# Optimization experiments

Measured on AMD Instinct MI355X. Metric: run time of the kernel, lower is better.

The kernel has to match this reference:

```python
import jax, jax.numpy as jnp
import numpy as np

N = 100000
E = 3200000
C = 32
EPS = 1e-5
SLOPE = 0.01  # nn.LeakyReLU default negative slope


def _param_key(i):
    return jax.random.fold_in(jax.random.key(42), i)


def setup_inputs() -> dict:
    key = jax.random.key(0)
    k0, k1, k2, k3 = jax.random.split(key, 4)
    patch_embs = jax.random.normal(k0, (N, C), jnp.float32)
    row = jax.random.randint(k1, (E,), 0, N)
    off = jax.random.randint(k2, (E,), 1, N)
    col = (row + off) % N  # guarantees no self loops (PyG removes+re-adds them)
    edge_index = jnp.stack([row, col]).astype(jnp.int64)
    edge_attr = jax.random.normal(k3, (E, 1), jnp.float32)
    s = 1.0 / np.sqrt(C)
    inp = {"patch_embs": patch_embs, "edge_index": edge_index, "edge_attr": edge_attr}
    for i in (1, 2, 3):
        ka, kb = jax.random.split(_param_key(i))
        inp[f"W{i}_out"] = jax.random.uniform(ka, (C, C), jnp.float32, -s, s)
        inp[f"b{i}_out"] = jnp.zeros((C,), jnp.float32)
        inp[f"W{i}_root"] = jax.random.uniform(kb, (C, C), jnp.float32, -s, s)
        inp[f"g{i}"] = jnp.ones((C,), jnp.float32)
        inp[f"be{i}"] = jnp.zeros((C,), jnp.float32)
    return inp


def _cluster_gcn(x, row, col, W_out, b_out, W_root):
    n = x.shape[0]
    loops = jnp.arange(n, dtype=row.dtype)
    r = jnp.concatenate([row, loops])
    c = jnp.concatenate([col, loops])
    deg = jax.ops.segment_sum(jnp.ones_like(c, jnp.float32), c, num_segments=n)
    deg_inv = 1.0 / jnp.clip(deg, 1.0)  # degree(col).clamp_(1.)
    w = deg_inv[c]  # diag_lambda = 0 default
    agg = jax.ops.segment_sum(x[r] * w[:, None], c, num_segments=n)
    return agg @ W_out + b_out + x @ W_root


def _bn_train(x, g, b):
    m = jnp.mean(x, axis=0)
    v = jnp.mean(jnp.square(x - m), axis=0)  # biased var, BatchNorm1d training
    return (x - m) * jax.lax.rsqrt(v + EPS) * g + b


def _leaky(x):
    return jnp.where(x >= 0, x, SLOPE * x)


def reference(patch_embs, edge_index, edge_attr,
              W1_out, b1_out, W1_root, g1, be1,
              W2_out, b2_out, W2_root, g2, be2,
              W3_out, b3_out, W3_root, g3, be3):
    row, col = edge_index[0], edge_index[1]
    x = _bn_train(_leaky(_cluster_gcn(patch_embs, row, col, W1_out, b1_out, W1_root)) + patch_embs, g1, be1)
    x = _bn_train(_leaky(_cluster_gcn(x, row, col, W2_out, b2_out, W2_root)) + x, g2, be2)
    x = _bn_train(_cluster_gcn(x, row, col, W3_out, b3_out, W3_root) + x, g3, be3)
    return x
```

## Files before the change

### kernel.cpp

```cpp
#include <hip/hip_runtime.h>
#include <hip/hip_fp8.h>

#define SLOPE 0.01f
#define BN_EPS 1e-5f
#define CH 32
#define GATHER_BLOCKS 3125
#define DENSE_BLOCKS 1024
#define APPLY_BLOCKS 1024
#define SLOTS 80

#define BSH 8
#define BNODES 256
#define NBMAX 512

#if defined(__has_builtin)
#if __has_builtin(__builtin_amdgcn_cvt_pk_f32_fp8)
#define USE_CVT_PK 1
#endif
#endif

typedef float v2f __attribute__((ext_vector_type(2)));
typedef float v4f __attribute__((ext_vector_type(4)));

static __device__ __forceinline__ float q2f(unsigned char b) {
    __hip_fp8_e4m3 t;
    t.__x = (__hip_fp8_storage_t)b;
    return (float)t;
}
static __device__ __forceinline__ unsigned char f2q(float f) {
    __hip_fp8_e4m3 t(f);
    return (unsigned char)t.__x;
}
static __device__ __forceinline__ unsigned short f2bf(float f) {
    unsigned int x = __float_as_uint(f);
    x += 0x7fffu + ((x >> 16) & 1u);
    return (unsigned short)(x >> 16);
}
static __device__ __forceinline__ float bf2f(unsigned int u16) {
    return __uint_as_float(u16 << 16);
}
static __device__ __forceinline__ void dec_add(unsigned int u, float4& a) {
#ifdef USE_CVT_PK
    v2f lo = __builtin_amdgcn_cvt_pk_f32_fp8((int)u, false);
    v2f hi = __builtin_amdgcn_cvt_pk_f32_fp8((int)u, true);
    a.x += lo.x; a.y += lo.y; a.z += hi.x; a.w += hi.y;
#else
    a.x += q2f((unsigned char)(u & 0xff));
    a.y += q2f((unsigned char)((u >> 8) & 0xff));
    a.z += q2f((unsigned char)((u >> 16) & 0xff));
    a.w += q2f((unsigned char)(u >> 24));
#endif
}
static __device__ __forceinline__ void nt_store4(const float4& a, float4* p) {
    v4f t; t.x = a.x; t.y = a.y; t.z = a.z; t.w = a.w;
    __builtin_nontemporal_store(t, (v4f*)p);
}

static __device__ __forceinline__ void fin_body(const float* __restrict__ partials,
        int nprt, const float* __restrict__ g, const float* __restrict__ be,
        float* __restrict__ stO, int nv) {
    __shared__ float4 red4[16][16];
    __shared__ double sdv[64];
    int tid = threadIdx.x;
    const float4* p4 = (const float4*)partials;
    int col4 = tid & 15, grp = tid >> 4;
    float4 s = make_float4(0.f, 0.f, 0.f, 0.f);
    for (int r = grp; r < nprt; r += 16) {
        float4 t = p4[(size_t)r * 16 + col4];
        s.x += t.x; s.y += t.y; s.z += t.z; s.w += t.w;
    }
    red4[grp][col4] = s;
    __syncthreads();
    if (tid < 64) {
        int c4 = tid >> 2, cc = tid & 3;
        double tot = 0.0;
#pragma unroll
        for (int k = 0; k < 16; ++k) {
            const float* rr = (const float*)&red4[k][c4];
            tot += (double)rr[cc];
        }
        sdv[tid] = tot;
    }
    __syncthreads();
    if (tid < 32) {
        double mean = sdv[tid] / (double)nv;
        double var  = sdv[32 + tid] / (double)nv - mean * mean;
        float inv = rsqrtf(fmaxf((float)var, 0.f) + BN_EPS);
        float scv = g[tid] * inv;
        stO[tid] = scv;
        stO[32 + tid] = be[tid] - (float)mean * scv;
    }
}


__global__ __launch_bounds__(256) void cast_hist_kernel(
        const float4* __restrict__ x4, unsigned int* __restrict__ xq4, int n4,
        const int* __restrict__ col, int* __restrict__ ghist, int nE, int nb,
        float* __restrict__ st0) {
    __shared__ int h[NBMAX];
    for (int i = threadIdx.x; i < nb; i += 256) h[i] = 0;
    __syncthreads();
    int gt = blockIdx.x * 256 + threadIdx.x, gs = gridDim.x * 256;
    for (int e = gt; e < nE; e += gs)
        atomicAdd(&h[col[e] >> BSH], 1);
    for (int i = gt; i < n4; i += gs) {
        float4 v = x4[i];
        unsigned int o = (unsigned int)f2q(v.x)
                       | ((unsigned int)f2q(v.y) << 8)
                       | ((unsigned int)f2q(v.z) << 16)
                       | ((unsigned int)f2q(v.w) << 24);
        xq4[i] = o;
    }
    if (blockIdx.x == 0) {
        if (threadIdx.x < 64)
            st0[threadIdx.x] = (threadIdx.x < 32) ? 1.0f : 0.0f;
        if (threadIdx.x < 8)
            xq4[n4 + threadIdx.x] = 0u;
    }
    __syncthreads();
    for (int i = threadIdx.x; i < nb; i += 256) {
        int v = h[i];
        if (v) atomicAdd(&ghist[i], v);
    }
}

__global__ __launch_bounds__(512) void bscan_kernel(const int* __restrict__ ghist,
        int* __restrict__ bbase, int* __restrict__ gcur, int nb) {
    __shared__ int sh[512];
    int tid = threadIdx.x;
    int v = (tid < nb) ? ghist[tid] : 0;
    sh[tid] = v;
    __syncthreads();
    int acc = v;
#pragma unroll
    for (int d = 1; d < 512; d <<= 1) {
        int t = (tid >= d) ? sh[tid - d] : 0;
        __syncthreads();
        acc += t;
        sh[tid] = acc;
        __syncthreads();
    }
    int excl = acc - v;
    if (tid < nb) { bbase[tid] = excl; gcur[tid] = excl; }
    if (tid == nb - 1) bbase[nb] = acc;
}

__global__ __launch_bounds__(1024) void part_kernel(const int* __restrict__ row,
        const int* __restrict__ col, int* __restrict__ gcur,
        unsigned int* __restrict__ staging, int nE, int nb) {
    __shared__ int hist[NBMAX], gb[NBMAX], lcur[NBMAX];
    int tid = threadIdx.x;
    for (int i = tid; i < nb; i += 1024) hist[i] = 0;
    __syncthreads();
    int base = blockIdx.x * 8192;
    int r[8], bk[8];
    unsigned int lo[8];
    bool ok[8];
#pragma unroll
    for (int k = 0; k < 8; ++k) {
        int e = base + (k << 10) + tid;
        ok[k] = (e < nE);
        if (ok[k]) {
            int rr = row[e], cc = col[e];
            r[k] = rr; bk[k] = cc >> BSH; lo[k] = (unsigned)(cc & (BNODES - 1));
            atomicAdd(&hist[bk[k]], 1);
        }
    }
    __syncthreads();
    for (int i = tid; i < nb; i += 1024) {
        int h = hist[i];
        if (h) gb[i] = atomicAdd(&gcur[i], h);
        lcur[i] = 0;
    }
    __syncthreads();
#pragma unroll
    for (int k = 0; k < 8; ++k) {
        if (ok[k]) {
            int b = bk[k];
            int p = gb[b] + atomicAdd(&lcur[b], 1);
            staging[p] = ((unsigned)r[k] << BSH) | lo[k];
        }
    }
}

__global__ __launch_bounds__(256) void build_kernel(const unsigned int* __restrict__ staging,
        const int* __restrict__ bbase, int* __restrict__ adj, int* __restrict__ pdeg,
        float* __restrict__ dinv, int n, int zoff) {
    int b = blockIdx.x;
    int b0 = b << BSH;
    int tid = threadIdx.x;
    int es = bbase[b], ee = bbase[b + 1];
    __shared__ int cnt[BNODES];
    cnt[tid] = 0;
    __syncthreads();
    for (int i = es + tid; i < ee; i += 256)
        atomicAdd(&cnt[staging[i] & (BNODES - 1)], 1);
    __syncthreads();
    int node = b0 + tid;
    int d = cnt[tid];
    if (node < n) {
        dinv[node] = 1.0f / (float)(d + 1);
        int pd = (d + 15) & ~15;
        if (pd > SLOTS) pd = SLOTS;
        pdeg[node] = pd;
        int ab = node * SLOTS;
        for (int s2 = d; s2 < pd; ++s2) adj[ab + s2] = zoff;
    }
    cnt[tid] = 0;
    __syncthreads();
    for (int i = es + tid; i < ee; i += 256) {
        unsigned int wv = staging[i];
        int c = wv & (BNODES - 1);
        int p = atomicAdd(&cnt[c], 1);
        if (p < SLOTS)
            adj[(b0 + c) * SLOTS + p] = (int)(wv >> BSH) * CH;
    }
}


__global__ __launch_bounds__(256, 4) void gather_kernel(
        const unsigned char* __restrict__ xq,
        const int* __restrict__ pdeg, const int* __restrict__ adj,
        float4* __restrict__ S4, int n,
        const float* __restrict__ partials, int nprt,
        const float* __restrict__ g, const float* __restrict__ be,
        float* __restrict__ st_out) {
    if (blockIdx.x >= GATHER_BLOCKS) {
        if (partials) fin_body(partials, nprt, g, be, st_out, n);
        return;
    }
    int tid = threadIdx.x;
    int lane = tid & 63, w = tid >> 6;
    int h = lane >> 5;
    int q = (lane & 31) >> 2;
    int r8 = (lane & 3) * 8;
    int half = (blockIdx.x * 4 + w) * 2 + h;
    int nH = GATHER_BLOCKS * 8;
    for (int base = half * 4; base < n; base += nH * 4) {
        int v0 = base, v1 = base + 1, v2 = base + 2, v3 = base + 3;
        int j0 = v0 * SLOTS, j1 = v1 * SLOTS, j2 = v2 * SLOTS, j3 = v3 * SLOTS;
        int e0 = j0 + pdeg[v0];
        int e1 = (v1 < n) ? j1 + pdeg[v1] : j1;
        int e2 = (v2 < n) ? j2 + pdeg[v2] : j2;
        int e3 = (v3 < n) ? j3 + pdeg[v3] : j3;
        float4 c0A = {0,0,0,0}, c0B = {0,0,0,0};
        float4 c1A = {0,0,0,0}, c1B = {0,0,0,0};
        float4 c2A = {0,0,0,0}, c2B = {0,0,0,0};
        float4 c3A = {0,0,0,0}, c3B = {0,0,0,0};
#define LD16(k) int aA##k = adj[j##k + q]; int aB##k = adj[j##k + 8 + q];
#define GD16(k) uint2 uA##k = *(const uint2*)(xq + aA##k + r8); \
                uint2 uB##k = *(const uint2*)(xq + aB##k + r8);
#define AC16(k) dec_add(uA##k.x, c##k##A); dec_add(uA##k.y, c##k##B); \
                dec_add(uB##k.x, c##k##A); dec_add(uB##k.y, c##k##B); j##k += 16;
        while (j0 < e0 && j1 < e1 && j2 < e2 && j3 < e3) {
            LD16(0) LD16(1) LD16(2) LD16(3)
            GD16(0) GD16(1) GD16(2) GD16(3)
            AC16(0) AC16(1) AC16(2) AC16(3)
        }
        while (j0 < e0 && j1 < e1) { LD16(0) LD16(1) GD16(0) GD16(1) AC16(0) AC16(1) }
        while (j2 < e2 && j3 < e3) { LD16(2) LD16(3) GD16(2) GD16(3) AC16(2) AC16(3) }
        while (j0 < e0) { LD16(0) GD16(0) AC16(0) }
        while (j1 < e1) { LD16(1) GD16(1) AC16(1) }
        while (j2 < e2) { LD16(2) GD16(2) AC16(2) }
        while (j3 < e3) { LD16(3) GD16(3) AC16(3) }
#undef LD16
#undef GD16
#undef AC16
#define MRG4(a, m) a.x += __shfl_xor(a.x, m); a.y += __shfl_xor(a.y, m); \
                   a.z += __shfl_xor(a.z, m); a.w += __shfl_xor(a.w, m);
        MRG4(c0A, 4)  MRG4(c0B, 4)  MRG4(c1A, 4)  MRG4(c1B, 4)
        MRG4(c2A, 4)  MRG4(c2B, 4)  MRG4(c3A, 4)  MRG4(c3B, 4)
        MRG4(c0A, 8)  MRG4(c0B, 8)  MRG4(c1A, 8)  MRG4(c1B, 8)
        MRG4(c2A, 8)  MRG4(c2B, 8)  MRG4(c3A, 8)  MRG4(c3B, 8)
        MRG4(c0A, 16) MRG4(c0B, 16) MRG4(c1A, 16) MRG4(c1B, 16)
        MRG4(c2A, 16) MRG4(c2B, 16) MRG4(c3A, 16) MRG4(c3B, 16)
#undef MRG4
        if (q == 0) {
            int r2 = r8 >> 2;
            nt_store4(c0A, &S4[(size_t)v0 * 8 + r2]);
            nt_store4(c0B, &S4[(size_t)v0 * 8 + r2 + 1]);
            if (v1 < n) { nt_store4(c1A, &S4[(size_t)v1 * 8 + r2]);
                          nt_store4(c1B, &S4[(size_t)v1 * 8 + r2 + 1]); }
            if (v2 < n) { nt_store4(c2A, &S4[(size_t)v2 * 8 + r2]);
                          nt_store4(c2B, &S4[(size_t)v2 * 8 + r2 + 1]); }
            if (v3 < n) { nt_store4(c3A, &S4[(size_t)v3 * 8 + r2]);
                          nt_store4(c3B, &S4[(size_t)v3 * 8 + r2 + 1]); }
        }
    }
}


__global__ __launch_bounds__(256) void dense_kernel(
        const float* __restrict__ zin, float* __restrict__ Sz,
        const float* __restrict__ dinv, const float* __restrict__ st,
        const float* __restrict__ Wout, const float* __restrict__ bout,
        const float* __restrict__ Wroot,
        float* __restrict__ partials, unsigned int* __restrict__ zq4,
        int n, int do_leaky) {
    __shared__ float2 WI[CH * CH];
    __shared__ float red[2][4][CH];
    int tid = threadIdx.x;
    for (int i = tid; i < CH * CH; i += 256)
        WI[i] = make_float2(Wout[i], Wroot[i]);
    __syncthreads();
    int lane = tid & 63, w = tid >> 6;
    int c = lane & 31, h = lane >> 5;
    float bo = bout[c];
    float sc = st[c], sh = st[32 + c];
    int hw0 = (blockIdx.x * 4 + w) * 2 + h;
    int nHW = gridDim.x * 8;
    float bsum = 0.f, bsq = 0.f;
    for (int v = hw0; v < n; v += nHW) {
        float Sv = Sz[(size_t)v * CH + c];
        float zv = zin[(size_t)v * CH + c];
        float xv = fmaf(sc, zv, sh);
        float a = fmaf(sc * (Sv + zv), dinv[v], sh);
        unsigned int pk = (unsigned int)f2bf(a) | ((unsigned int)f2bf(xv) << 16);
        float2 acc0 = {0.f, 0.f}, acc1 = {0.f, 0.f};
        float2 acc2 = {0.f, 0.f}, acc3 = {0.f, 0.f};
#pragma unroll
        for (int k = 0; k < CH; k += 4) {
            unsigned int p0 = __shfl(pk, k,     32);
            unsigned int p1 = __shfl(pk, k + 1, 32);
            unsigned int p2 = __shfl(pk, k + 2, 32);
            unsigned int p3 = __shfl(pk, k + 3, 32);
            float2 w0 = WI[k * CH + c];
            float2 w1 = WI[(k + 1) * CH + c];
            float2 w2 = WI[(k + 2) * CH + c];
            float2 w3 = WI[(k + 3) * CH + c];
            acc0.x += bf2f(p0 & 0xffffu) * w0.x; acc0.y += bf2f(p0 >> 16) * w0.y;
            acc1.x += bf2f(p1 & 0xffffu) * w1.x; acc1.y += bf2f(p1 >> 16) * w1.y;
            acc2.x += bf2f(p2 & 0xffffu) * w2.x; acc2.y += bf2f(p2 >> 16) * w2.y;
            acc3.x += bf2f(p3 & 0xffffu) * w3.x; acc3.y += bf2f(p3 >> 16) * w3.y;
        }
        float y = ((acc0.x + acc0.y) + (acc1.x + acc1.y))
                + ((acc2.x + acc2.y) + (acc3.x + acc3.y)) + bo;
        float zz = do_leaky ? (y >= 0.f ? y : SLOPE * y) : y;
        zz += xv;
        Sz[(size_t)v * CH + c] = zz;
        bsum += zz; bsq += zz * zz;
        if (zq4) {
            unsigned int b0 = (unsigned int)f2q(zz);
            unsigned int b1 = __shfl_down(b0, 1, 32);
            unsigned int b2 = __shfl_down(b0, 2, 32);
            unsigned int b3 = __shfl_down(b0, 3, 32);
            if ((c & 3) == 0)
                zq4[(size_t)v * 8 + (c >> 2)] = b0 | (b1 << 8) | (b2 << 16) | (b3 << 24);
        }
    }
    bsum += __shfl_xor(bsum, 32);
    bsq  += __shfl_xor(bsq, 32);
    if (h == 0) { red[0][w][c] = bsum; red[1][w][c] = bsq; }
    __syncthreads();
    if (tid < 64) {
        int which = tid >> 5, cc = tid & 31;
        float sv = red[which][0][cc] + red[which][1][cc] + red[which][2][cc] + red[which][3][cc];
        partials[blockIdx.x * 64 + which * 32 + cc] = sv;
    }
}


__global__ __launch_bounds__(256) void fin_kernel(const float* __restrict__ partials,
        int nprt, const float* __restrict__ g, const float* __restrict__ be,
        float* __restrict__ stO, int nv) {
    fin_body(partials, nprt, g, be, stO, nv);
}

__global__ __launch_bounds__(256) void bn_apply_kernel(const float4* __restrict__ z4,
        const float* __restrict__ st, float4* __restrict__ xout, int n4) {
    __shared__ float sL[64];
    if (threadIdx.x < 64) sL[threadIdx.x] = st[threadIdx.x];
    __syncthreads();
    for (int i = blockIdx.x * blockDim.x + threadIdx.x; i < n4; i += gridDim.x * blockDim.x) {
        float4 zz = z4[i];
        int c0 = (i & 7) * 4;
        float4 o;
        o.x = zz.x * sL[c0]     + sL[32 + c0];
        o.y = zz.y * sL[c0 + 1] + sL[32 + c0 + 1];
        o.z = zz.z * sL[c0 + 2] + sL[32 + c0 + 2];
        o.w = zz.w * sL[c0 + 3] + sL[32 + c0 + 3];
        xout[i] = o;
    }
}


extern "C" void kernel_launch(void* const* d_in, const int* in_sizes, int n_in,
                              void* d_out, int out_size, void* d_ws, size_t ws_size,
                              hipStream_t stream) {
    const float* x0 = (const float*)d_in[0];
    const int* ei = (const int*)d_in[1];
    int nE = in_sizes[1] / 2;
    int n = in_sizes[0] / CH;
    const int* row = ei;
    const int* col = ei + nE;
    const float* W_out[3]  = {(const float*)d_in[3],  (const float*)d_in[8],  (const float*)d_in[13]};
    const float* b_out[3]  = {(const float*)d_in[4],  (const float*)d_in[9],  (const float*)d_in[14]};
    const float* W_root[3] = {(const float*)d_in[5],  (const float*)d_in[10], (const float*)d_in[15]};
    const float* gam[3]    = {(const float*)d_in[6],  (const float*)d_in[11], (const float*)d_in[16]};
    const float* bet[3]    = {(const float*)d_in[7],  (const float*)d_in[12], (const float*)d_in[17]};

    int nb = (n + BNODES - 1) >> BSH;

    char* w = (char*)d_ws;
    auto carve = [&](size_t bytes) { char* p = w; w += (bytes + 511) & ~511ull; return p; };
    int*   adj     = (int*)  carve((size_t)n * SLOTS * 4);
    int*   pdeg    = (int*)  carve((size_t)n * 4);
    float* dinv    = (float*)carve((size_t)n * 4);
    int*   ghist   = (int*)  carve((size_t)NBMAX * 4);
    int*   bbase   = (int*)  carve((size_t)(NBMAX + 1) * 4);
    int*   gcur    = (int*)  carve((size_t)NBMAX * 4);
    size_t zbytes  = (size_t)n * CH * 4;
    size_t sbytes  = (size_t)nE * 4;
    char*  uni     = (char*) carve(zbytes > sbytes ? zbytes : sbytes);
    unsigned int* staging = (unsigned int*)uni;
    float* bufA    = (float*)uni;
    float* bufB    = (float*)carve(zbytes);
    unsigned char* xq = (unsigned char*)carve((size_t)(n + 1) * CH);
    float* parts   = (float*)carve((size_t)DENSE_BLOCKS * 64 * 4);
    float* stb     = (float*)carve((size_t)4 * 64 * 4);

    hipMemsetAsync(ghist, 0, (size_t)NBMAX * 4, stream);
    int n4 = n * CH / 4;
    cast_hist_kernel<<<1024, 256, 0, stream>>>((const float4*)x0, (unsigned int*)xq, n4,
            col, ghist, nE, nb, stb);
    bscan_kernel<<<1, 512, 0, stream>>>(ghist, bbase, gcur, nb);
    int pb = (nE + 8191) / 8192;
    part_kernel<<<pb, 1024, 0, stream>>>(row, col, gcur, staging, nE, nb);
    build_kernel<<<nb, 256, 0, stream>>>(staging, bbase, adj, pdeg, dinv, n, n * CH);

    gather_kernel<<<GATHER_BLOCKS + 1, 256, 0, stream>>>(xq, pdeg, adj, (float4*)bufA, n,
            nullptr, 0, nullptr, nullptr, nullptr);
    dense_kernel<<<DENSE_BLOCKS, 256, 0, stream>>>(x0, bufA, dinv, stb,
            W_out[0], b_out[0], W_root[0], parts, (unsigned int*)xq, n, 1);
    gather_kernel<<<GATHER_BLOCKS + 1, 256, 0, stream>>>(xq, pdeg, adj, (float4*)bufB, n,
            parts, DENSE_BLOCKS, gam[0], bet[0], stb + 64);
    dense_kernel<<<DENSE_BLOCKS, 256, 0, stream>>>(bufA, bufB, dinv, stb + 64,
            W_out[1], b_out[1], W_root[1], parts, (unsigned int*)xq, n, 1);
    gather_kernel<<<GATHER_BLOCKS + 1, 256, 0, stream>>>(xq, pdeg, adj, (float4*)bufA, n,
            parts, DENSE_BLOCKS, gam[1], bet[1], stb + 128);
    dense_kernel<<<DENSE_BLOCKS, 256, 0, stream>>>(bufB, bufA, dinv, stb + 128,
            W_out[2], b_out[2], W_root[2], parts, nullptr, n, 0);
    fin_kernel<<<1, 256, 0, stream>>>(parts, DENSE_BLOCKS, gam[2], bet[2], stb + 192, n);
    bn_apply_kernel<<<APPLY_BLOCKS, 256, 0, stream>>>((const float4*)bufA, stb + 192,
            (float4*)d_out, n4);
}
```

Before: 308.2 us.

## Restructure gather to preload adjacency via shuffles and software-pipeline fp8 row loads

```diff
diff --git a/kernel.cpp b/kernel.cpp
--- a/kernel.cpp
+++ b/kernel.cpp
@@ -4,7 +4,7 @@
 #define SLOPE 0.01f
 #define BN_EPS 1e-5f
 #define CH 32
-#define GATHER_BLOCKS 3125
+#define GATHER_BLOCKS 6250
 #define DENSE_BLOCKS 1024
 #define APPLY_BLOCKS 1024
 #define SLOTS 80
@@ -218,7 +218,7 @@
 }
 
 
-__global__ __launch_bounds__(256, 4) void gather_kernel(
+__global__ __launch_bounds__(256) void gather_kernel(
         const unsigned char* __restrict__ xq,
         const int* __restrict__ pdeg, const int* __restrict__ adj,
         float4* __restrict__ S4, int n,
@@ -231,60 +231,78 @@
     }
     int tid = threadIdx.x;
     int lane = tid & 63, w = tid >> 6;
-    int h = lane >> 5;
-    int q = (lane & 31) >> 2;
-    int r8 = (lane & 3) * 8;
-    int half = (blockIdx.x * 4 + w) * 2 + h;
-    int nH = GATHER_BLOCKS * 8;
-    for (int base = half * 4; base < n; base += nH * 4) {
-        int v0 = base, v1 = base + 1, v2 = base + 2, v3 = base + 3;
-        int j0 = v0 * SLOTS, j1 = v1 * SLOTS, j2 = v2 * SLOTS, j3 = v3 * SLOTS;
-        int e0 = j0 + pdeg[v0];
-        int e1 = (v1 < n) ? j1 + pdeg[v1] : j1;
-        int e2 = (v2 < n) ? j2 + pdeg[v2] : j2;
-        int e3 = (v3 < n) ? j3 + pdeg[v3] : j3;
-        float4 c0A = {0,0,0,0}, c0B = {0,0,0,0};
-        float4 c1A = {0,0,0,0}, c1B = {0,0,0,0};
-        float4 c2A = {0,0,0,0}, c2B = {0,0,0,0};
-        float4 c3A = {0,0,0,0}, c3B = {0,0,0,0};
-#define LD16(k) int aA##k = adj[j##k + q]; int aB##k = adj[j##k + 8 + q];
-#define GD16(k) uint2 uA##k = *(const uint2*)(xq + aA##k + r8); \
-                uint2 uB##k = *(const uint2*)(xq + aB##k + r8);
-#define AC16(k) dec_add(uA##k.x, c##k##A); dec_add(uA##k.y, c##k##B); \
-                dec_add(uB##k.x, c##k##A); dec_add(uB##k.y, c##k##B); j##k += 16;
-        while (j0 < e0 && j1 < e1 && j2 < e2 && j3 < e3) {
-            LD16(0) LD16(1) LD16(2) LD16(3)
-            GD16(0) GD16(1) GD16(2) GD16(3)
-            AC16(0) AC16(1) AC16(2) AC16(3)
-        }
-        while (j0 < e0 && j1 < e1) { LD16(0) LD16(1) GD16(0) GD16(1) AC16(0) AC16(1) }
-        while (j2 < e2 && j3 < e3) { LD16(2) LD16(3) GD16(2) GD16(3) AC16(2) AC16(3) }
-        while (j0 < e0) { LD16(0) GD16(0) AC16(0) }
-        while (j1 < e1) { LD16(1) GD16(1) AC16(1) }
-        while (j2 < e2) { LD16(2) GD16(2) AC16(2) }
-        while (j3 < e3) { LD16(3) GD16(3) AC16(3) }
-#undef LD16
-#undef GD16
-#undef AC16
-#define MRG4(a, m) a.x += __shfl_xor(a.x, m); a.y += __shfl_xor(a.y, m); \
-                   a.z += __shfl_xor(a.z, m); a.w += __shfl_xor(a.w, m);
-        MRG4(c0A, 4)  MRG4(c0B, 4)  MRG4(c1A, 4)  MRG4(c1B, 4)
-        MRG4(c2A, 4)  MRG4(c2B, 4)  MRG4(c3A, 4)  MRG4(c3B, 4)
-        MRG4(c0A, 8)  MRG4(c0B, 8)  MRG4(c1A, 8)  MRG4(c1B, 8)
-        MRG4(c2A, 8)  MRG4(c2B, 8)  MRG4(c3A, 8)  MRG4(c3B, 8)
-        MRG4(c0A, 16) MRG4(c0B, 16) MRG4(c1A, 16) MRG4(c1B, 16)
-        MRG4(c2A, 16) MRG4(c2B, 16) MRG4(c3A, 16) MRG4(c3B, 16)
+    int h = lane >> 5, l32 = lane & 31;
+    int q = l32 >> 2;
+    int r8 = (l32 & 3) * 8;
+    int zoff = n * CH;
+    int half0 = (blockIdx.x * 4 + w) * 2 + h;
+    int nstride = GATHER_BLOCKS * 8 * 2;
+    for (int v0 = half0 * 2; v0 < n; v0 += nstride) {
+        int v1 = v0 + 1;
+        int pd0 = pdeg[v0];
+        int pd1 = (v1 < n) ? pdeg[v1] : 0;
+        size_t ab0 = (size_t)v0 * SLOTS;
+        size_t ab1 = (size_t)(v1 < n ? v1 : v0) * SLOTS;
+        int a00 = adj[ab0 + l32];
+        int a10 = adj[ab1 + l32];
+        int a01 = (pd0 > 32) ? adj[ab0 + 32 + l32] : zoff;
+        int a11 = (pd1 > 32) ? adj[ab1 + 32 + l32] : zoff;
+        int a02 = (pd0 > 64) ? adj[ab0 + 64 + l32] : zoff;
+        int a12 = (pd1 > 64) ? adj[ab1 + 64 + l32] : zoff;
+        a00 = (l32      < pd0) ? a00 : zoff;
+        a01 = (l32 + 32 < pd0) ? a01 : zoff;
+        a02 = (l32 + 64 < pd0) ? a02 : zoff;
+        a10 = (l32      < pd1) ? a10 : zoff;
+        a11 = (l32 + 32 < pd1) ? a11 : zoff;
+        a12 = (l32 + 64 < pd1) ? a12 : zoff;
+        int m = pd0 > pd1 ? pd0 : pd1;
+        int mo = __shfl_xor(m, 32);
+        m = m > mo ? m : mo;
+        int nbatch = m >> 4;
+        float4 A0 = {0,0,0,0}, B0 = {0,0,0,0};
+        float4 A1 = {0,0,0,0}, B1 = {0,0,0,0};
+        if (nbatch > 0) {
+            int eA0 = __shfl(a00, q, 32),     eB0 = __shfl(a00, q + 8, 32);
+            int eA1 = __shfl(a10, q, 32),     eB1 = __shfl(a10, q + 8, 32);
+            uint2 uA0 = *(const uint2*)(xq + eA0 + r8);
+            uint2 uB0 = *(const uint2*)(xq + eB0 + r8);
+            uint2 uA1 = *(const uint2*)(xq + eA1 + r8);
+            uint2 uB1 = *(const uint2*)(xq + eB1 + r8);
+            for (int b = 1; b < nbatch; ++b) {
+                int rg0 = (b >= 4) ? a02 : ((b >= 2) ? a01 : a00);
+                int rg1 = (b >= 4) ? a12 : ((b >= 2) ? a11 : a10);
+                int s = ((b & 1) << 4) + q;
+                int nA0 = __shfl(rg0, s, 32), nB0 = __shfl(rg0, s + 8, 32);
+                int nA1 = __shfl(rg1, s, 32), nB1 = __shfl(rg1, s + 8, 32);
+                uint2 vA0 = *(const uint2*)(xq + nA0 + r8);
+                uint2 vB0 = *(const uint2*)(xq + nB0 + r8);
+                uint2 vA1 = *(const uint2*)(xq + nA1 + r8);
+                uint2 vB1 = *(const uint2*)(xq + nB1 + r8);
+                dec_add(uA0.x, A0); dec_add(uA0.y, B0);
+                dec_add(uB0.x, A0); dec_add(uB0.y, B0);
+                dec_add(uA1.x, A1); dec_add(uA1.y, B1);
+                dec_add(uB1.x, A1); dec_add(uB1.y, B1);
+                uA0 = vA0; uB0 = vB0; uA1 = vA1; uB1 = vB1;
+            }
+            dec_add(uA0.x, A0); dec_add(uA0.y, B0);
+            dec_add(uB0.x, A0); dec_add(uB0.y, B0);
+            dec_add(uA1.x, A1); dec_add(uA1.y, B1);
+            dec_add(uB1.x, A1); dec_add(uB1.y, B1);
+        }
+#define MRG4(a, mk) a.x += __shfl_xor(a.x, mk); a.y += __shfl_xor(a.y, mk); \
+                    a.z += __shfl_xor(a.z, mk); a.w += __shfl_xor(a.w, mk);
+        MRG4(A0, 4)  MRG4(B0, 4)  MRG4(A1, 4)  MRG4(B1, 4)
+        MRG4(A0, 8)  MRG4(B0, 8)  MRG4(A1, 8)  MRG4(B1, 8)
+        MRG4(A0, 16) MRG4(B0, 16) MRG4(A1, 16) MRG4(B1, 16)
 #undef MRG4
         if (q == 0) {
             int r2 = r8 >> 2;
-            nt_store4(c0A, &S4[(size_t)v0 * 8 + r2]);
-            nt_store4(c0B, &S4[(size_t)v0 * 8 + r2 + 1]);
-            if (v1 < n) { nt_store4(c1A, &S4[(size_t)v1 * 8 + r2]);
-                          nt_store4(c1B, &S4[(size_t)v1 * 8 + r2 + 1]); }
-            if (v2 < n) { nt_store4(c2A, &S4[(size_t)v2 * 8 + r2]);
-                          nt_store4(c2B, &S4[(size_t)v2 * 8 + r2 + 1]); }
-            if (v3 < n) { nt_store4(c3A, &S4[(size_t)v3 * 8 + r2]);
-                          nt_store4(c3B, &S4[(size_t)v3 * 8 + r2 + 1]); }
+            nt_store4(A0, &S4[(size_t)v0 * 8 + r2]);
+            nt_store4(B0, &S4[(size_t)v0 * 8 + r2 + 1]);
+            if (v1 < n) {
+                nt_store4(A1, &S4[(size_t)v1 * 8 + r2]);
+                nt_store4(B1, &S4[(size_t)v1 * 8 + r2 + 1]);
+            }
         }
     }
 }
@@ -403,7 +421,7 @@
 
     char* w = (char*)d_ws;
     auto carve = [&](size_t bytes) { char* p = w; w += (bytes + 511) & ~511ull; return p; };
-    int*   adj     = (int*)  carve((size_t)n * SLOTS * 4);
+    int*   adj     = (int*)  carve((size_t)n * SLOTS * 4 + 1024);
     int*   pdeg    = (int*)  carve((size_t)n * 4);
     float* dinv    = (float*)carve((size_t)n * 4);
     int*   ghist   = (int*)  carve((size_t)NBMAX * 4);
```

Measured after the change: 299.9 us. -2.7%, faster.
